# Kernel optimization log

Measured on AMD Instinct MI355X. Metric: run time of the kernel, lower is better.

The kernel has to match this reference:

```python
import jax, jax.numpy as jnp
import numpy as np


def _grid_sample_3d(src, grid):
    """Trilinear grid_sample, align_corners=True, zero padding.
    src: [B,C,D,H,W], grid: [B,D,H,W,3] with last dim (x,y,z) ~ (W,H,D) in [-1,1].
    """
    B, C, D, H, W = src.shape
    gx, gy, gz = grid[..., 0], grid[..., 1], grid[..., 2]
    # unnormalize (align_corners=True): -1 -> 0, +1 -> dim-1
    ix = (gx + 1.0) * ((W - 1) / 2.0)
    iy = (gy + 1.0) * ((H - 1) / 2.0)
    iz = (gz + 1.0) * ((D - 1) / 2.0)
    ix0 = jnp.floor(ix); iy0 = jnp.floor(iy); iz0 = jnp.floor(iz)
    fx = ix - ix0; fy = iy - iy0; fz = iz - iz0  # fractional parts
    x0 = ix0.astype(jnp.int32); y0 = iy0.astype(jnp.int32); z0 = iz0.astype(jnp.int32)

    src_flat = src.reshape(B, C, D * H * W)
    out = jnp.zeros((B, C, D * H * W), dtype=src.dtype)
    for dz in (0, 1):
        for dy in (0, 1):
            for dx in (0, 1):
                xc = x0 + dx; yc = y0 + dy; zc = z0 + dz
                w = ((fx if dx else 1.0 - fx)
                     * (fy if dy else 1.0 - fy)
                     * (fz if dz else 1.0 - fz))
                valid = ((xc >= 0) & (xc < W) & (yc >= 0) & (yc < H)
                         & (zc >= 0) & (zc < D))
                xs = jnp.clip(xc, 0, W - 1)
                ys = jnp.clip(yc, 0, H - 1)
                zs = jnp.clip(zc, 0, D - 1)
                lin = ((zs * H + ys) * W + xs).reshape(B, -1)  # [B, DHW]
                vals = jax.vmap(lambda s, i: jnp.take(s, i, axis=1))(src_flat, lin)  # [B,C,DHW]
                out = out + (w * valid).reshape(B, 1, -1).astype(src.dtype) * vals
    return out.reshape(B, C, D, H, W)


def _affine_grid_3d(theta, D, H, W):
    """torch affine_grid (align_corners=True) for size [B,3,D,H,W]. Returns [B,D,H,W,3]."""
    xs = jnp.linspace(-1.0, 1.0, W, dtype=theta.dtype)
    ys = jnp.linspace(-1.0, 1.0, H, dtype=theta.dtype)
    zs = jnp.linspace(-1.0, 1.0, D, dtype=theta.dtype)
    bx = jnp.broadcast_to(xs[None, None, :], (D, H, W))
    by = jnp.broadcast_to(ys[None, :, None], (D, H, W))
    bz = jnp.broadcast_to(zs[:, None, None], (D, H, W))
    base = jnp.stack([bx, by, bz, jnp.ones((D, H, W), theta.dtype)], axis=-1)  # [D,H,W,4]
    return jnp.einsum('bij,dhwj->bdhwi', theta, base)


def setup_inputs() -> dict:
    key = jax.random.key(0)
    k1, k2 = jax.random.split(key)
    B, C, D, H, W = 2, 2, 160, 192, 224
    src = jax.random.normal(k1, (B, C, D, H, W), dtype=jnp.float32)
    eye = jnp.concatenate([jnp.eye(3, dtype=jnp.float32),
                           jnp.zeros((3, 1), jnp.float32)], axis=1)  # [3,4]
    mat = eye[None] + 0.05 * jax.random.normal(k2, (B, 3, 4), dtype=jnp.float32)
    return {"src": src, "mat": mat}


def reference(src, mat):
    B, C, D, H, W = src.shape
    norm = jnp.array([[1, 1, 1, D], [1, 1, 1, H], [1, 1, 1, W]], dtype=mat.dtype)
    theta = mat / norm[None]  # normalize translation column by spatial dims
    grid = _affine_grid_3d(theta, D, H, W)
    return _grid_sample_3d(src, grid)
```

## Files before the change

### kernel.cpp

```cpp
#include <hip/hip_runtime.h>

#define BB 2
#define CC 2
#define DD 160
#define HH 192
#define WW 224
#define DHW (DD * HH * WW)

#define VPT 4
#define TPB 256
#define NBX (DHW / (TPB * VPT))
#define NXCD 8
#define CPX (NBX / NXCD)

typedef float f2v __attribute__((ext_vector_type(2)));
typedef float f4v __attribute__((ext_vector_type(4)));

__device__ __forceinline__ f2v load2u(const float* p) {
    struct __attribute__((packed)) S { f2v v; };
    return ((const S*)p)->v;
}

__global__ __launch_bounds__(TPB) void affine_sample_kernel(
    const float* __restrict__ src,
    const float* __restrict__ mat,
    float* __restrict__ out)
{
    int bx  = blockIdx.x;
    int sbx = (bx & (NXCD - 1)) * CPX + (bx >> 3);
    int base = (sbx * TPB + (int)threadIdx.x) * VPT;
    int b = blockIdx.y;

    int w = base % WW;
    int t = base / WW;
    int h = t % HH;
    int d = t / HH;

    const float* m = mat + b * 12;
    float a00 = m[0], a01 = m[1], a02 = m[2],  a03 = m[3]  * (1.0f / (float)DD);
    float a10 = m[4], a11 = m[5], a12 = m[6],  a13 = m[7]  * (1.0f / (float)HH);
    float a20 = m[8], a21 = m[9], a22 = m[10], a23 = m[11] * (1.0f / (float)WW);

    float xn = -1.0f + (float)w * (2.0f / (float)(WW - 1));
    float yn = -1.0f + (float)h * (2.0f / (float)(HH - 1));
    float zn = -1.0f + (float)d * (2.0f / (float)(DD - 1));

    float ix = (a00 * xn + a01 * yn + a02 * zn + a03 + 1.0f) * ((float)(WW - 1) * 0.5f);
    float iy = (a10 * xn + a11 * yn + a12 * zn + a13 + 1.0f) * ((float)(HH - 1) * 0.5f);
    float iz = (a20 * xn + a21 * yn + a22 * zn + a23 + 1.0f) * ((float)(DD - 1) * 0.5f);

    float dix = a00;
    float diy = a10 * ((float)(HH - 1) / (float)(WW - 1));
    float diz = a20 * ((float)(DD - 1) / (float)(WW - 1));

    const float* sb = src + (size_t)b * (CC * DHW);

    f2v   P0[VPT][4], P1[VPT][4];
    float q0a[VPT], q1a[VPT];
    float wzy0[VPT], wzy1[VPT], wzy2[VPT], wzy3[VPT];

    #pragma unroll
    for (int v = 0; v < VPT; ++v) {
        float ixv = fmaf((float)v, dix, ix);
        float iyv = fmaf((float)v, diy, iy);
        float izv = fmaf((float)v, diz, iz);

        float fx0 = floorf(ixv), fy0 = floorf(iyv), fz0 = floorf(izv);
        float fx = ixv - fx0, fy = iyv - fy0, fz = izv - fz0;
        int x0 = (int)fx0, y0 = (int)fy0, z0 = (int)fz0;
        int x1 = x0 + 1, y1 = y0 + 1, z1 = z0 + 1;

        float wx0 = (x0 >= 0 && x0 < WW) ? (1.0f - fx) : 0.0f;
        float wx1 = (x1 >= 0 && x1 < WW) ? fx          : 0.0f;
        float wy0 = (y0 >= 0 && y0 < HH) ? (1.0f - fy) : 0.0f;
        float wy1 = (y1 >= 0 && y1 < HH) ? fy          : 0.0f;
        float wz0 = (z0 >= 0 && z0 < DD) ? (1.0f - fz) : 0.0f;
        float wz1 = (z1 >= 0 && z1 < DD) ? fz          : 0.0f;

        int xc0 = min(max(x0, 0), WW - 1), xc1 = min(max(x1, 0), WW - 1);
        int yc0 = min(max(y0, 0), HH - 1), yc1 = min(max(y1, 0), HH - 1);
        int zc0 = min(max(z0, 0), DD - 1), zc1 = min(max(z1, 0), DD - 1);

        int xb   = min(xc0, WW - 2);
        int sel0 = xc0 - xb;
        int sel1 = xc1 - xb;

        q0a[v] = (sel0 ? 0.0f : wx0) + (sel1 ? 0.0f : wx1);
        q1a[v] = (sel0 ? wx0 : 0.0f) + (sel1 ? wx1 : 0.0f);

        wzy0[v] = wz0 * wy0; wzy1[v] = wz0 * wy1;
        wzy2[v] = wz1 * wy0; wzy3[v] = wz1 * wy1;

        int zh0 = zc0 * HH, zh1 = zc1 * HH;
        int r0 = (zh0 + yc0) * WW + xb;
        int r1 = (zh0 + yc1) * WW + xb;
        int r2 = (zh1 + yc0) * WW + xb;
        int r3 = (zh1 + yc1) * WW + xb;

        P0[v][0] = load2u(sb + r0);
        P0[v][1] = load2u(sb + r1);
        P0[v][2] = load2u(sb + r2);
        P0[v][3] = load2u(sb + r3);
        P1[v][0] = load2u(sb + (DHW + r0));
        P1[v][1] = load2u(sb + (DHW + r1));
        P1[v][2] = load2u(sb + (DHW + r2));
        P1[v][3] = load2u(sb + (DHW + r3));
    }

    f4v o0, o1;
    #pragma unroll
    for (int v = 0; v < VPT; ++v) {
        float rq00 = wzy0[v] * q0a[v], rq01 = wzy0[v] * q1a[v];
        float rq10 = wzy1[v] * q0a[v], rq11 = wzy1[v] * q1a[v];
        float rq20 = wzy2[v] * q0a[v], rq21 = wzy2[v] * q1a[v];
        float rq30 = wzy3[v] * q0a[v], rq31 = wzy3[v] * q1a[v];

        o0[v] = rq00 * P0[v][0][0] + rq01 * P0[v][0][1]
              + rq10 * P0[v][1][0] + rq11 * P0[v][1][1]
              + rq20 * P0[v][2][0] + rq21 * P0[v][2][1]
              + rq30 * P0[v][3][0] + rq31 * P0[v][3][1];
        o1[v] = rq00 * P1[v][0][0] + rq01 * P1[v][0][1]
              + rq10 * P1[v][1][0] + rq11 * P1[v][1][1]
              + rq20 * P1[v][2][0] + rq21 * P1[v][2][1]
              + rq30 * P1[v][3][0] + rq31 * P1[v][3][1];
    }

    float* ob = out + (size_t)b * (CC * DHW) + base;
    __builtin_nontemporal_store(o0, (f4v*)ob);
    __builtin_nontemporal_store(o1, (f4v*)(ob + DHW));
}

extern "C" void kernel_launch(void* const* d_in, const int* in_sizes, int n_in,
                              void* d_out, int out_size, void* d_ws, size_t ws_size,
                              hipStream_t stream) {
    const float* src = (const float*)d_in[0];
    const float* mat = (const float*)d_in[1];
    float* out = (float*)d_out;

    dim3 block(TPB);
    dim3 grid(NBX, BB);
    affine_sample_kernel<<<grid, block, 0, stream>>>(src, mat, out);
}
```

Measured before the change: 281.1 us.

## Assign each thread outputs strided across depth quarters instead of consecutive x

Each thread now computes four outputs spaced a quarter of the depth apart rather than four adjacent x positions. Adjacent lanes therefore handle adjacent x, so their gather loads and their scalar output stores are coalesced across the wavefront. The change also adds a sched_barrier to keep all loads issued before the math, and sets a launch-bounds occupancy hint of 4. In exchange it gives up the 128-bit vector stores and the x-direction locality that a single thread had across its own four samples.

```diff
diff --git a/kernel.cpp b/kernel.cpp
--- a/kernel.cpp
+++ b/kernel.cpp
@@ -8,27 +8,28 @@
 #define DHW (DD * HH * WW)
 
 #define VPT 4
+#define QD  (DD / VPT)
+#define QOFF (QD * HH * WW)
 #define TPB 256
-#define NBX (DHW / (TPB * VPT))
+#define NBX (QOFF / TPB)
 #define NXCD 8
 #define CPX (NBX / NXCD)
 
 typedef float f2v __attribute__((ext_vector_type(2)));
-typedef float f4v __attribute__((ext_vector_type(4)));
 
 __device__ __forceinline__ f2v load2u(const float* p) {
     struct __attribute__((packed)) S { f2v v; };
     return ((const S*)p)->v;
 }
 
-__global__ __launch_bounds__(TPB) void affine_sample_kernel(
+__global__ __launch_bounds__(TPB, 4) void affine_sample_kernel(
     const float* __restrict__ src,
     const float* __restrict__ mat,
     float* __restrict__ out)
 {
     int bx  = blockIdx.x;
     int sbx = (bx & (NXCD - 1)) * CPX + (bx >> 3);
-    int base = (sbx * TPB + (int)threadIdx.x) * VPT;
+    int base = sbx * TPB + (int)threadIdx.x;
     int b = blockIdx.y;
 
     int w = base % WW;
@@ -49,11 +50,13 @@
     float iy = (a10 * xn + a11 * yn + a12 * zn + a13 + 1.0f) * ((float)(HH - 1) * 0.5f);
     float iz = (a20 * xn + a21 * yn + a22 * zn + a23 + 1.0f) * ((float)(DD - 1) * 0.5f);
 
-    float dix = a00;
-    float diy = a10 * ((float)(HH - 1) / (float)(WW - 1));
-    float diz = a20 * ((float)(DD - 1) / (float)(WW - 1));
+    float dzn = (float)QD * (2.0f / (float)(DD - 1));
+    float dix = a02 * dzn * ((float)(WW - 1) * 0.5f);
+    float diy = a12 * dzn * ((float)(HH - 1) * 0.5f);
+    float diz = a22 * dzn * ((float)(DD - 1) * 0.5f);
 
-    const float* sb = src + (size_t)b * (CC * DHW);
+    const float* s0 = src + (size_t)b * (CC * DHW);
+    const float* s1 = s0 + DHW;
 
     f2v   P0[VPT][4], P1[VPT][4];
     float q0a[VPT], q1a[VPT];
@@ -97,17 +100,19 @@
         int r2 = (zh1 + yc0) * WW + xb;
         int r3 = (zh1 + yc1) * WW + xb;
 
-        P0[v][0] = load2u(sb + r0);
-        P0[v][1] = load2u(sb + r1);
-        P0[v][2] = load2u(sb + r2);
-        P0[v][3] = load2u(sb + r3);
-        P1[v][0] = load2u(sb + (DHW + r0));
-        P1[v][1] = load2u(sb + (DHW + r1));
-        P1[v][2] = load2u(sb + (DHW + r2));
-        P1[v][3] = load2u(sb + (DHW + r3));
+        P0[v][0] = load2u(s0 + r0);
+        P0[v][1] = load2u(s0 + r1);
+        P0[v][2] = load2u(s0 + r2);
+        P0[v][3] = load2u(s0 + r3);
+        P1[v][0] = load2u(s1 + r0);
+        P1[v][1] = load2u(s1 + r1);
+        P1[v][2] = load2u(s1 + r2);
+        P1[v][3] = load2u(s1 + r3);
     }
 
-    f4v o0, o1;
+    __builtin_amdgcn_sched_barrier(0);
+
+    float* o = out + (size_t)b * (CC * DHW) + base;
     #pragma unroll
     for (int v = 0; v < VPT; ++v) {
         float rq00 = wzy0[v] * q0a[v], rq01 = wzy0[v] * q1a[v];
@@ -115,19 +120,18 @@
         float rq20 = wzy2[v] * q0a[v], rq21 = wzy2[v] * q1a[v];
         float rq30 = wzy3[v] * q0a[v], rq31 = wzy3[v] * q1a[v];
 
-        o0[v] = rq00 * P0[v][0][0] + rq01 * P0[v][0][1]
-              + rq10 * P0[v][1][0] + rq11 * P0[v][1][1]
-              + rq20 * P0[v][2][0] + rq21 * P0[v][2][1]
-              + rq30 * P0[v][3][0] + rq31 * P0[v][3][1];
-        o1[v] = rq00 * P1[v][0][0] + rq01 * P1[v][0][1]
-              + rq10 * P1[v][1][0] + rq11 * P1[v][1][1]
-              + rq20 * P1[v][2][0] + rq21 * P1[v][2][1]
-              + rq30 * P1[v][3][0] + rq31 * P1[v][3][1];
+        float acc0 = rq00 * P0[v][0][0] + rq01 * P0[v][0][1]
+                   + rq10 * P0[v][1][0] + rq11 * P0[v][1][1]
+                   + rq20 * P0[v][2][0] + rq21 * P0[v][2][1]
+                   + rq30 * P0[v][3][0] + rq31 * P0[v][3][1];
+        float acc1 = rq00 * P1[v][0][0] + rq01 * P1[v][0][1]
+                   + rq10 * P1[v][1][0] + rq11 * P1[v][1][1]
+                   + rq20 * P1[v][2][0] + rq21 * P1[v][2][1]
+                   + rq30 * P1[v][3][0] + rq31 * P1[v][3][1];
+
+        __builtin_nontemporal_store(acc0, o + v * QOFF);
+        __builtin_nontemporal_store(acc1, o + (DHW + v * QOFF));
     }
-
-    float* ob = out + (size_t)b * (CC * DHW) + base;
-    __builtin_nontemporal_store(o0, (f4v*)ob);
-    __builtin_nontemporal_store(o1, (f4v*)(ob + DHW));
 }
 
 extern "C" void kernel_launch(void* const* d_in, const int* in_sizes, int n_in,
```

After: 243.7 us. 13.3% less time.
